# Kernel tuning notes

Hardware: AMD Instinct MI355X
Metric: run time of the kernel (lower is better)

## Reference

```python
import jax, jax.numpy as jnp
import numpy as np
import math

B, N, H, D = 2, 2048, 16, 64

def setup_inputs() -> dict:
    key = jax.random.key(0)
    kq, kk, kv = jax.random.split(key, 3)
    q = jax.random.normal(kq, (B, N, H, D), dtype=jnp.float32)
    k = jax.random.normal(kk, (B, N, H, D), dtype=jnp.float32)
    v = jax.random.normal(kv, (B, N, H, D), dtype=jnp.float32)
    return {"q": q, "k": k, "v": v}

def reference(q, k, v):
    d = q.shape[-1]
    # [b,n,h,d] -> [b,h,n,d]
    qh = jnp.transpose(q, (0, 2, 1, 3))
    kh = jnp.transpose(k, (0, 2, 1, 3))
    vh = jnp.transpose(v, (0, 2, 1, 3))
    # scores: [b,h,n,n]
    scores = jnp.einsum('bhqd,bhkd->bhqk', qh, kh) / math.sqrt(d)
    # jax.nn.softmax performs the stable max-subtraction internally,
    # matching the original's explicit max-subtract + softmax.
    attn = jax.nn.softmax(scores, axis=-1)
    o = jnp.einsum('bhqk,bhkd->bhqd', attn, vh)
    # back to [b,n,h,d]
    return jnp.transpose(o, (0, 2, 1, 3))
```

## Files before the change

kernel.cpp:

```cpp
#include <hip/hip_runtime.h>


typedef float  f32x4  __attribute__((ext_vector_type(4)));
typedef float  f32x16 __attribute__((ext_vector_type(16)));
typedef short  s16x8  __attribute__((ext_vector_type(8)));
typedef short  s16x4  __attribute__((ext_vector_type(4)));
typedef int    i32x4  __attribute__((ext_vector_type(4)));

#define QSCALE 0.18033688011112042f

__device__ __forceinline__ unsigned short bf16r(float f) {
    unsigned u = __builtin_bit_cast(unsigned, f);
    u += 0x7fffu + ((u >> 16) & 1u);
    return (unsigned short)(u >> 16);
}

__device__ __forceinline__ s16x8 cvt8f_scaled(const float* p, float s) {
    f32x4 a = *(const f32x4*)p;
    f32x4 b = *(const f32x4*)(p + 4);
    s16x8 r;
#pragma unroll
    for (int i = 0; i < 4; ++i) {
        r[i]   = (short)bf16r(a[i] * s);
        r[i+4] = (short)bf16r(b[i] * s);
    }
    return r;
}

__device__ __forceinline__ int cvtpk2(float lo, float hi) {
    int r;
    asm("v_cvt_pk_bf16_f32 %0, %1, %2" : "=v"(r) : "v"(lo), "v"(hi));
    return r;
}

__global__ void __launch_bounds__(256)
prep(const float* __restrict__ K, const float* __restrict__ V,
     unsigned short* __restrict__ Kt, unsigned short* __restrict__ Vt) {
    const int t = threadIdx.x, bid = blockIdx.x;
    const int bh = bid & 31, nb = bid >> 5;
    const int b = bh >> 4, h = bh & 15;
    const size_t tile0 = ((size_t)bh * 64 + nb * 2) * 2048;

#pragma unroll
    for (int i = 0; i < 2; ++i) {
        const int lin = i * 256 + t;
        const int kbl = lin >> 8, rem = lin & 255;
        const int kc = rem >> 6, l = rem & 63;
        const int nl = l & 31, gg = l >> 5;
        const float* src = K + ((size_t)(b * 2048 + nb * 64 + kbl * 32 + nl)) * 1024
                             + h * 64 + kc * 16 + gg * 8;
        f32x4 a = *(const f32x4*)src;
        f32x4 c = *(const f32x4*)(src + 4);
        i32x4 o = { cvtpk2(a[0], a[1]), cvtpk2(a[2], a[3]),
                    cvtpk2(c[0], c[1]), cvtpk2(c[2], c[3]) };
        *(i32x4*)(Kt + tile0 + kbl * 2048 + kc * 512 + l * 8) = o;
    }

#pragma unroll
    for (int i = 0; i < 2; ++i) {
        const int lin = i * 256 + t;
        const int kbl = lin >> 8, rem = lin & 255;
        const int qq = rem >> 6, l = rem & 63;
        const int dt = qq >> 1, s = qq & 1;
        const int nl = l & 31, gg = l >> 5;
        const float* vp0 = V + ((size_t)(b * 2048 + nb * 64 + kbl * 32 + 8 * s + 4 * gg)) * 1024
                             + h * 64 + dt * 32 + nl;
        float x0 = vp0[0],     x1 = vp0[1024],  x2 = vp0[2048],  x3 = vp0[3072];
        float x4 = vp0[16384], x5 = vp0[17408], x6 = vp0[18432], x7 = vp0[19456];
        i32x4 o = { cvtpk2(x0, x1), cvtpk2(x2, x3),
                    cvtpk2(x4, x5), cvtpk2(x6, x7) };
        *(i32x4*)(Vt + tile0 + kbl * 2048 + qq * 512 + l * 8) = o;
    }
}

__global__ void __launch_bounds__(256, 3)
attn_fwd(const float* __restrict__ Q, const unsigned short* __restrict__ Kt,
         const unsigned short* __restrict__ Vt, float* __restrict__ O)
{
    __shared__ __align__(16) float ex[3 * 64 * 36];

    const int t = threadIdx.x;
    const int ksel = t >> 6, lane = t & 63;
    const int g = lane >> 5, nl = lane & 31;

    const int bid = blockIdx.x;
    const int bh  = bid & 31, qb = bid >> 5;
    const int b   = bh >> 4,  h  = bh & 15;
    const int q0  = qb * 32;

    s16x8 qf[4];
    {
        const float* qp = Q + ((size_t)(b * 2048 + q0 + nl)) * 1024 + h * 64 + g * 8;
#pragma unroll
        for (int kc = 0; kc < 4; ++kc)
            qf[kc] = cvt8f_scaled(qp + kc * 16, QSCALE);
    }

    const unsigned short* kp = Kt + (size_t)bh * 131072 + (size_t)ksel * 32768 + lane * 8;
    const unsigned short* vp = Vt + (size_t)bh * 131072 + (size_t)ksel * 32768 + lane * 8;

    f32x16 oa0 = {}, oa1 = {};
    f32x4  lpv = {};

    s16x8 kfa[4], vfa[4], kfb[4], vfb[4];

#define LOADT(KD, VD, IT) do {                                              \
        const unsigned short* _k = kp + (IT) * 2048;                        \
        const unsigned short* _v = vp + (IT) * 2048;                        \
        _Pragma("unroll")                                                   \
        for (int _i = 0; _i < 4; ++_i) {                                    \
            KD[_i] = *(const s16x8*)(_k + _i * 512);                        \
            VD[_i] = *(const s16x8*)(_v + _i * 512);                        \
        } } while (0)

#define STEP(KF, VF) do {                                                   \
        f32x16 sacc = {};                                                   \
        _Pragma("unroll")                                                   \
        for (int _kc = 0; _kc < 4; ++_kc)                                   \
            sacc = __builtin_amdgcn_mfma_f32_32x32x16_bf16(                 \
                KF[_kc], qf[_kc], sacc, 0, 0, 0);                           \
        int pk[8];                                                          \
        _Pragma("unroll")                                                   \
        for (int _c = 0; _c < 4; ++_c) {                                    \
            f32x4 e = { __builtin_amdgcn_exp2f(sacc[4*_c]),                 \
                        __builtin_amdgcn_exp2f(sacc[4*_c+1]),               \
                        __builtin_amdgcn_exp2f(sacc[4*_c+2]),               \
                        __builtin_amdgcn_exp2f(sacc[4*_c+3]) };             \
            lpv += e;                                                       \
            pk[2*_c]   = cvtpk2(e[0], e[1]);                                \
            pk[2*_c+1] = cvtpk2(e[2], e[3]);                                \
        }                                                                   \
        _Pragma("unroll")                                                   \
        for (int _s = 0; _s < 2; ++_s) {                                    \
            i32x4 bd = { pk[_s*2], pk[_s*2+1], pk[_s*2+4], pk[_s*2+5] };    \
            s16x8 bb = __builtin_bit_cast(s16x8, bd);                       \
            oa0 = __builtin_amdgcn_mfma_f32_32x32x16_bf16(VF[_s],     bb, oa0, 0, 0, 0); \
            oa1 = __builtin_amdgcn_mfma_f32_32x32x16_bf16(VF[2 + _s], bb, oa1, 0, 0, 0); \
        } } while (0)

    LOADT(kfa, vfa, 0);
    LOADT(kfb, vfb, 1);
#pragma unroll
    for (int it = 0; it < 16; ++it) {
        __builtin_amdgcn_sched_barrier(0);
        if ((it & 1) == 0) {
            STEP(kfa, vfa);
            if (it + 2 < 16) LOADT(kfa, vfa, it + 2);
        } else {
            STEP(kfb, vfb);
            if (it + 2 < 16) LOADT(kfb, vfb, it + 2);
        }
    }
    __builtin_amdgcn_sched_barrier(0);
#undef LOADT
#undef STEP

    const float lp = lpv[0] + lpv[1] + lpv[2] + lpv[3];

    if (ksel) {
        float* zone = ex + (ksel - 1) * 2304 + lane * 36;
#pragma unroll
        for (int i = 0; i < 4; ++i) {
            *(f32x4*)(zone + i * 4) =
                (f32x4){ oa0[4*i], oa0[4*i+1], oa0[4*i+2], oa0[4*i+3] };
            *(f32x4*)(zone + 16 + i * 4) =
                (f32x4){ oa1[4*i], oa1[4*i+1], oa1[4*i+2], oa1[4*i+3] };
        }
        zone[32] = lp;
    }
    __syncthreads();
    if (!ksel) {
        float lps = lp;
#pragma unroll
        for (int z = 0; z < 3; ++z) {
            const float* zn = ex + z * 2304 + lane * 36;
#pragma unroll
            for (int i = 0; i < 4; ++i) {
                f32x4 u0 = *(const f32x4*)(zn + i * 4);
                f32x4 u1 = *(const f32x4*)(zn + 16 + i * 4);
#pragma unroll
                for (int j = 0; j < 4; ++j) { oa0[4*i+j] += u0[j]; oa1[4*i+j] += u1[j]; }
            }
            lps += zn[32];
        }
        float ssum = lps + __shfl_xor(lps, 32);
        const float inv = 1.0f / ssum;
        float* op = O + ((size_t)(b * 2048 + q0 + nl)) * 1024 + h * 64;
#pragma unroll
        for (int rq = 0; rq < 4; ++rq) {
            const int d0 = 8 * rq + 4 * g;
            *(f32x4*)(op + d0) = (f32x4){
                oa0[4*rq]   * inv, oa0[4*rq+1] * inv,
                oa0[4*rq+2] * inv, oa0[4*rq+3] * inv };
            *(f32x4*)(op + 32 + d0) = (f32x4){
                oa1[4*rq]   * inv, oa1[4*rq+1] * inv,
                oa1[4*rq+2] * inv, oa1[4*rq+3] * inv };
        }
    }
}

extern "C" void kernel_launch(void* const* d_in, const int* in_sizes, int n_in,
                              void* d_out, int out_size, void* d_ws, size_t ws_size,
                              hipStream_t stream) {
    const float* q = (const float*)d_in[0];
    const float* k = (const float*)d_in[1];
    const float* v = (const float*)d_in[2];
    float* o = (float*)d_out;

    unsigned short* Kt = (unsigned short*)d_ws;
    unsigned short* Vt = Kt + 4194304;

    hipLaunchKernelGGL(prep,     dim3(1024), dim3(256), 0, stream, k, v, Kt, Vt);
    hipLaunchKernelGGL(attn_fwd, dim3(2048), dim3(256), 0, stream, q, Kt, Vt, o);
}
```

Before: 137.9 us.

## Process 64 queries per wave and split keys across two waves

Each block now covers 128 queries. Each wave computes two 32-query tiles against half of the key range, so every K/V fragment loaded feeds twice as many MFMAs, and the 4-way key split becomes a 2-way split with a smaller LDS reduction. The grid shrinks from 2048 to 512 blocks and the occupancy hint drops from 3 to 2 blocks per CU to make room for the larger register footprint. The main loop is no longer fully unrolled. The trade is less global/L2 traffic for K/V against fewer blocks in flight and higher register pressure.

```diff
diff --git a/kernel.cpp b/kernel.cpp
--- a/kernel.cpp
+++ b/kernel.cpp
@@ -73,128 +73,158 @@
     }
 }
 
-__global__ void __launch_bounds__(256, 3)
+__global__ void __launch_bounds__(256, 2)
 attn_fwd(const float* __restrict__ Q, const unsigned short* __restrict__ Kt,
          const unsigned short* __restrict__ Vt, float* __restrict__ O)
 {
-    __shared__ __align__(16) float ex[3 * 64 * 36];
+    __shared__ __align__(16) float ex[2 * 64 * 68];
 
     const int t = threadIdx.x;
-    const int ksel = t >> 6, lane = t & 63;
+    const int w = t >> 6, lane = t & 63;
     const int g = lane >> 5, nl = lane & 31;
+    const int qsel = w & 1, ksel = w >> 1;
 
     const int bid = blockIdx.x;
     const int bh  = bid & 31, qb = bid >> 5;
     const int b   = bh >> 4,  h  = bh & 15;
-    const int q0  = qb * 32;
-
-    s16x8 qf[4];
-    {
-        const float* qp = Q + ((size_t)(b * 2048 + q0 + nl)) * 1024 + h * 64 + g * 8;
+    const int q0  = qb * 128 + qsel * 64;
+
+    s16x8 qf[2][4];
+#pragma unroll
+    for (int qt = 0; qt < 2; ++qt) {
+        const float* qp = Q + ((size_t)(b * 2048 + q0 + qt * 32 + nl)) * 1024
+                            + h * 64 + g * 8;
 #pragma unroll
         for (int kc = 0; kc < 4; ++kc)
-            qf[kc] = cvt8f_scaled(qp + kc * 16, QSCALE);
-    }
-
-    const unsigned short* kp = Kt + (size_t)bh * 131072 + (size_t)ksel * 32768 + lane * 8;
-    const unsigned short* vp = Vt + (size_t)bh * 131072 + (size_t)ksel * 32768 + lane * 8;
-
-    f32x16 oa0 = {}, oa1 = {};
-    f32x4  lpv = {};
+            qf[qt][kc] = cvt8f_scaled(qp + kc * 16, QSCALE);
+    }
+
+    const unsigned short* ka = Kt + (size_t)bh * 131072 + (size_t)ksel * 65536 + lane * 8;
+    const unsigned short* va = Vt + (size_t)bh * 131072 + (size_t)ksel * 65536 + lane * 8;
+
+    f32x16 oa00 = {}, oa01 = {}, oa10 = {}, oa11 = {};
+    f32x4  lpv0 = {}, lpv1 = {};
 
     s16x8 kfa[4], vfa[4], kfb[4], vfb[4];
 
-#define LOADT(KD, VD, IT) do {                                              \
-        const unsigned short* _k = kp + (IT) * 2048;                        \
-        const unsigned short* _v = vp + (IT) * 2048;                        \
+#define LOADT(KD, VD) do {                                                  \
         _Pragma("unroll")                                                   \
         for (int _i = 0; _i < 4; ++_i) {                                    \
-            KD[_i] = *(const s16x8*)(_k + _i * 512);                        \
-            VD[_i] = *(const s16x8*)(_v + _i * 512);                        \
-        } } while (0)
-
-#define STEP(KF, VF) do {                                                   \
+            KD[_i] = *(const s16x8*)(ka + _i * 512);                        \
+            VD[_i] = *(const s16x8*)(va + _i * 512);                        \
+        }                                                                   \
+        ka += 2048; va += 2048; } while (0)
+
+#define QKROW(KF, QFq, LPV, PK) do {                                        \
         f32x16 sacc = {};                                                   \
         _Pragma("unroll")                                                   \
         for (int _kc = 0; _kc < 4; ++_kc)                                   \
             sacc = __builtin_amdgcn_mfma_f32_32x32x16_bf16(                 \
-                KF[_kc], qf[_kc], sacc, 0, 0, 0);                           \
-        int pk[8];                                                          \
+                KF[_kc], QFq[_kc], sacc, 0, 0, 0);                          \
         _Pragma("unroll")                                                   \
         for (int _c = 0; _c < 4; ++_c) {                                    \
             f32x4 e = { __builtin_amdgcn_exp2f(sacc[4*_c]),                 \
                         __builtin_amdgcn_exp2f(sacc[4*_c+1]),               \
                         __builtin_amdgcn_exp2f(sacc[4*_c+2]),               \
                         __builtin_amdgcn_exp2f(sacc[4*_c+3]) };             \
-            lpv += e;                                                       \
-            pk[2*_c]   = cvtpk2(e[0], e[1]);                                \
-            pk[2*_c+1] = cvtpk2(e[2], e[3]);                                \
-        }                                                                   \
+            LPV += e;                                                       \
+            PK[2*_c]   = cvtpk2(e[0], e[1]);                                \
+            PK[2*_c+1] = cvtpk2(e[2], e[3]);                                \
+        } } while (0)
+
+#define STEP(KF, VF) do {                                                   \
+        int pk0[8], pk1[8];                                                 \
+        QKROW(KF, qf[0], lpv0, pk0);                                        \
+        QKROW(KF, qf[1], lpv1, pk1);                                        \
         _Pragma("unroll")                                                   \
         for (int _s = 0; _s < 2; ++_s) {                                    \
-            i32x4 bd = { pk[_s*2], pk[_s*2+1], pk[_s*2+4], pk[_s*2+5] };    \
-            s16x8 bb = __builtin_bit_cast(s16x8, bd);                       \
-            oa0 = __builtin_amdgcn_mfma_f32_32x32x16_bf16(VF[_s],     bb, oa0, 0, 0, 0); \
-            oa1 = __builtin_amdgcn_mfma_f32_32x32x16_bf16(VF[2 + _s], bb, oa1, 0, 0, 0); \
+            i32x4 b0 = { pk0[_s*2], pk0[_s*2+1], pk0[_s*2+4], pk0[_s*2+5] };\
+            i32x4 b1 = { pk1[_s*2], pk1[_s*2+1], pk1[_s*2+4], pk1[_s*2+5] };\
+            s16x8 bb0 = __builtin_bit_cast(s16x8, b0);                      \
+            s16x8 bb1 = __builtin_bit_cast(s16x8, b1);                      \
+            oa00 = __builtin_amdgcn_mfma_f32_32x32x16_bf16(VF[_s],     bb0, oa00, 0, 0, 0); \
+            oa10 = __builtin_amdgcn_mfma_f32_32x32x16_bf16(VF[2 + _s], bb0, oa10, 0, 0, 0); \
+            oa01 = __builtin_amdgcn_mfma_f32_32x32x16_bf16(VF[_s],     bb1, oa01, 0, 0, 0); \
+            oa11 = __builtin_amdgcn_mfma_f32_32x32x16_bf16(VF[2 + _s], bb1, oa11, 0, 0, 0); \
         } } while (0)
 
-    LOADT(kfa, vfa, 0);
-    LOADT(kfb, vfb, 1);
-#pragma unroll
-    for (int it = 0; it < 16; ++it) {
+    LOADT(kfa, vfa);
+    LOADT(kfb, vfb);
+
+    for (int n = 0; n < 15; ++n) {
         __builtin_amdgcn_sched_barrier(0);
-        if ((it & 1) == 0) {
-            STEP(kfa, vfa);
-            if (it + 2 < 16) LOADT(kfa, vfa, it + 2);
-        } else {
-            STEP(kfb, vfb);
-            if (it + 2 < 16) LOADT(kfb, vfb, it + 2);
-        }
+        STEP(kfa, vfa);
+        LOADT(kfa, vfa);
+        __builtin_amdgcn_sched_barrier(0);
+        STEP(kfb, vfb);
+        LOADT(kfb, vfb);
     }
     __builtin_amdgcn_sched_barrier(0);
+    STEP(kfa, vfa);
+    STEP(kfb, vfb);
+
 #undef LOADT
+#undef QKROW
 #undef STEP
 
-    const float lp = lpv[0] + lpv[1] + lpv[2] + lpv[3];
-
+    float lp[2] = { lpv0[0] + lpv0[1] + lpv0[2] + lpv0[3],
+                    lpv1[0] + lpv1[1] + lpv1[2] + lpv1[3] };
+
+    __syncthreads();
+    float* zone = ex + qsel * (64 * 68) + lane * 68;
     if (ksel) {
-        float* zone = ex + (ksel - 1) * 2304 + lane * 36;
 #pragma unroll
         for (int i = 0; i < 4; ++i) {
             *(f32x4*)(zone + i * 4) =
-                (f32x4){ oa0[4*i], oa0[4*i+1], oa0[4*i+2], oa0[4*i+3] };
+                (f32x4){ oa00[4*i], oa00[4*i+1], oa00[4*i+2], oa00[4*i+3] };
             *(f32x4*)(zone + 16 + i * 4) =
-                (f32x4){ oa1[4*i], oa1[4*i+1], oa1[4*i+2], oa1[4*i+3] };
-        }
-        zone[32] = lp;
+                (f32x4){ oa01[4*i], oa01[4*i+1], oa01[4*i+2], oa01[4*i+3] };
+            *(f32x4*)(zone + 32 + i * 4) =
+                (f32x4){ oa10[4*i], oa10[4*i+1], oa10[4*i+2], oa10[4*i+3] };
+            *(f32x4*)(zone + 48 + i * 4) =
+                (f32x4){ oa11[4*i], oa11[4*i+1], oa11[4*i+2], oa11[4*i+3] };
+        }
+        zone[64] = lp[0];
+        zone[65] = lp[1];
     }
     __syncthreads();
     if (!ksel) {
-        float lps = lp;
-#pragma unroll
-        for (int z = 0; z < 3; ++z) {
-            const float* zn = ex + z * 2304 + lane * 36;
-#pragma unroll
-            for (int i = 0; i < 4; ++i) {
-                f32x4 u0 = *(const f32x4*)(zn + i * 4);
-                f32x4 u1 = *(const f32x4*)(zn + 16 + i * 4);
-#pragma unroll
-                for (int j = 0; j < 4; ++j) { oa0[4*i+j] += u0[j]; oa1[4*i+j] += u1[j]; }
+#pragma unroll
+        for (int i = 0; i < 4; ++i) {
+            f32x4 u0 = *(const f32x4*)(zone + i * 4);
+            f32x4 u1 = *(const f32x4*)(zone + 16 + i * 4);
+            f32x4 u2 = *(const f32x4*)(zone + 32 + i * 4);
+            f32x4 u3 = *(const f32x4*)(zone + 48 + i * 4);
+#pragma unroll
+            for (int j = 0; j < 4; ++j) {
+                oa00[4*i+j] += u0[j]; oa01[4*i+j] += u1[j];
+                oa10[4*i+j] += u2[j]; oa11[4*i+j] += u3[j];
             }
-            lps += zn[32];
-        }
-        float ssum = lps + __shfl_xor(lps, 32);
-        const float inv = 1.0f / ssum;
-        float* op = O + ((size_t)(b * 2048 + q0 + nl)) * 1024 + h * 64;
+        }
+        float inv[2];
+#pragma unroll
+        for (int qt = 0; qt < 2; ++qt) {
+            float s = lp[qt] + zone[64 + qt];
+            s += __shfl_xor(s, 32);
+            inv[qt] = 1.0f / s;
+        }
+        float* op0 = O + ((size_t)(b * 2048 + q0 + nl)) * 1024 + h * 64;
+        float* op1 = op0 + 32 * 1024;
 #pragma unroll
         for (int rq = 0; rq < 4; ++rq) {
             const int d0 = 8 * rq + 4 * g;
-            *(f32x4*)(op + d0) = (f32x4){
-                oa0[4*rq]   * inv, oa0[4*rq+1] * inv,
-                oa0[4*rq+2] * inv, oa0[4*rq+3] * inv };
-            *(f32x4*)(op + 32 + d0) = (f32x4){
-                oa1[4*rq]   * inv, oa1[4*rq+1] * inv,
-                oa1[4*rq+2] * inv, oa1[4*rq+3] * inv };
+            *(f32x4*)(op0 + d0) = (f32x4){
+                oa00[4*rq]   * inv[0], oa00[4*rq+1] * inv[0],
+                oa00[4*rq+2] * inv[0], oa00[4*rq+3] * inv[0] };
+            *(f32x4*)(op0 + 32 + d0) = (f32x4){
+                oa10[4*rq]   * inv[0], oa10[4*rq+1] * inv[0],
+                oa10[4*rq+2] * inv[0], oa10[4*rq+3] * inv[0] };
+            *(f32x4*)(op1 + d0) = (f32x4){
+                oa01[4*rq]   * inv[1], oa01[4*rq+1] * inv[1],
+                oa01[4*rq+2] * inv[1], oa01[4*rq+3] * inv[1] };
+            *(f32x4*)(op1 + 32 + d0) = (f32x4){
+                oa11[4*rq]   * inv[1], oa11[4*rq+1] * inv[1],
+                oa11[4*rq+2] * inv[1], oa11[4*rq+3] * inv[1] };
         }
     }
 }
@@ -211,5 +241,5 @@
     unsigned short* Vt = Kt + 4194304;
 
     hipLaunchKernelGGL(prep,     dim3(1024), dim3(256), 0, stream, k, v, Kt, Vt);
-    hipLaunchKernelGGL(attn_fwd, dim3(2048), dim3(256), 0, stream, q, Kt, Vt, o);
-}
+    hipLaunchKernelGGL(attn_fwd, dim3(512),  dim3(256), 0, stream, q, Kt, Vt, o);
+}
```

Measured after the change: 127.5 us. 1.08x faster.
